# Kernel optimization log

Measured on AMD Instinct MI355X. Metric: run time of the kernel, lower is better.

Reference implementation:

```python
import jax, jax.numpy as jnp
import numpy as np

SENSOR_H, SENSOR_W = 256, 256
SPP = 16
BATCH, C, H_IMG, W_IMG = 4, 3, 1024, 1024


def setup_inputs() -> dict:
    key = jax.random.key(0)
    k1, k2 = jax.random.split(key)
    img = jax.random.uniform(k1, (BATCH, C, H_IMG, W_IMG), dtype=jnp.float32)
    jitter = jax.random.uniform(k2, (SPP, SENSOR_H, SENSOR_W, 2), dtype=jnp.float32)
    t = jnp.ones((1,), jnp.float32)
    return {"img": img, "t": t, "jitter": jitter}


def deform(pos, t):
    # Analytic per-axis foveation diffeomorphism [-1,1]^2 -> [-1,1]^2:
    #   f(u) = tanh(t*u)/tanh(t), f'(u) = t*(1 - tanh(t*u)^2)/tanh(t)
    # Jacobian is diagonal, so det = f'(x) * f'(y).
    tt = t[0]
    s = jnp.tanh(tt)
    th = jnp.tanh(tt * pos)
    warped = th / s                      # (..., 2)
    dd = tt * (1.0 - th * th) / s        # diagonal Jacobian entries (..., 2)
    det = dd[..., 0] * dd[..., 1]        # (...)
    return warped, det


def grid_sample_border(img, grid):
    # img: (b,c,H,W); grid: (spp,h,w,2) in [-1,1]
    # bilinear, padding_mode='border', align_corners=False (matches F.grid_sample)
    b, c, H, W = img.shape
    gx = (grid[..., 0] + 1.0) * (W / 2.0) - 0.5
    gy = (grid[..., 1] + 1.0) * (H / 2.0) - 0.5
    gx = jnp.clip(gx, 0.0, W - 1.0)
    gy = jnp.clip(gy, 0.0, H - 1.0)
    x0 = jnp.floor(gx)
    y0 = jnp.floor(gy)
    wx = (gx - x0)[None, None]           # (1,1,spp,h,w)
    wy = (gy - y0)[None, None]
    x0i = jnp.clip(x0.astype(jnp.int32), 0, W - 1)
    y0i = jnp.clip(y0.astype(jnp.int32), 0, H - 1)
    x1i = jnp.clip(x0i + 1, 0, W - 1)
    y1i = jnp.clip(y0i + 1, 0, H - 1)
    # fancy-index gather: result (b,c,spp,h,w); avoids tiling img over (b*spp)
    v00 = img[:, :, y0i, x0i]
    v01 = img[:, :, y0i, x1i]
    v10 = img[:, :, y1i, x0i]
    v11 = img[:, :, y1i, x1i]
    return (v00 * (1 - wx) * (1 - wy) + v01 * wx * (1 - wy)
            + v10 * (1 - wx) * wy + v11 * wx * wy)


def reference(img, t, jitter):
    step_x = 2.0 / SENSOR_W
    step_y = 2.0 / SENSOR_H
    px = jnp.arange(-1.0, 1.0, step_x, dtype=jnp.float32)
    py = jnp.arange(-1.0, 1.0, step_y, dtype=jnp.float32)
    gx, gy = jnp.meshgrid(px, py, indexing='xy')          # (h, w)
    pixel_pos = jnp.stack((gx, gy), axis=-1)[None]        # (1, h, w, 2)
    jit = jitter * jnp.array([step_x, step_y], jnp.float32)
    pos = pixel_pos + jit                                 # (spp, h, w, 2)
    warped, det = deform(pos, t)                          # (spp,h,w,2), (spp,h,w)
    samples = grid_sample_border(img, warped)             # (b, c, spp, h, w)
    weighted = jnp.mean(samples * det[None, None], axis=2)  # (b, c, h, w)
    area = jnp.mean(det, axis=0)[None, None]              # (1, 1, h, w)
    return weighted / area
```

## Files before the change

### kernel.cpp

```cpp
#include <hip/hip_runtime.h>
#include <hip/hip_fp16.h>

#define SPP   16
#define SH    256
#define SW    256
#define HI    1024
#define WI    1024
#define CH    3
#define BATCH 4

#define TS    4
#define MAXD  26
#define PLN   704
#define NITER 11
#define NTHR  128

#define AS1C(p) ((const __attribute__((address_space(1))) void*)(p))
#define AS3(p)  ((__attribute__((address_space(3))) void*)(p))

__device__ __forceinline__ float fast_tanh(float x) {
    const float e = __expf(2.0f * x);
    return (e - 1.0f) * __builtin_amdgcn_rcpf(e + 1.0f);
}

__global__ __launch_bounds__(NTHR, 6) void foveated_async4(
    const float* __restrict__ img,
    const float* __restrict__ t_ptr,
    const float* __restrict__ jitter,
    float* __restrict__ out)
{
    __shared__ float lds_f[2][CH][PLN];

    const int bid  = blockIdx.x;
    const int Lb   = (bid & 7) * 1024 + (bid >> 3);
    const int th   = threadIdx.x;
    const int w    = th >> 6;
    const int lane = th & 63;

    const int tile = Lb * 2 + w;
    const int b    = tile >> 12;
    const int rem  = tile & 4095;
    const int trow = rem >> 6;
    const int tcol = rem & 63;
    const int sx0  = tcol * TS;
    const int sy0  = trow * TS;

    const float step  = 2.0f / 256.0f;
    const float tt    = t_ptr[0];
    const float inv_s = __builtin_amdgcn_rcpf(fast_tanh(tt));

    auto gmap = [&](float p) {
        float g = (fast_tanh(tt * p) * inv_s + 1.0f) * 512.0f - 0.5f;
        return fminf(fmaxf(g, 0.0f), 1023.0f);
    };
    const float pxmin = -1.0f + sx0 * step, pxmax = pxmin + TS * step;
    const float pymin = -1.0f + sy0 * step, pymax = pymin + TS * step;
    const int x_lo = max((int)gmap(pxmin) - 1, 0);
    const int x_hi = min((int)gmap(pxmax) + 2, WI - 1);
    const int y_lo = max((int)gmap(pymin) - 1, 0);
    const int y_hi = min((int)gmap(pymax) + 2, HI - 1);
    const int ncols = x_hi - x_lo + 1;
    const int nrows = y_hi - y_lo + 1;
    const bool fits = (ncols > 0) && (nrows > 0) &&
                      (ncols <= MAXD) && (nrows <= MAXD);

    const size_t plane = (size_t)HI * WI;
    const float* __restrict__ p0 = img + (size_t)(b * CH) * plane;
    const float* __restrict__ p1 = p0 + plane;
    const float* __restrict__ p2 = p1 + plane;

    const int p  = lane >> 2;
    const int q  = lane & 3;
    const int sx = sx0 + (p & 3);
    const int sy = sy0 + (p >> 2);

    const float px = -1.0f + sx * step;
    const float py = -1.0f + sy * step;

    const float2* __restrict__ jit2 = (const float2*)jitter;
    const int jbase = (q * 4) * (SH * SW) + sy * SW + sx;
    const float2 jv0 = jit2[jbase];
    const float2 jv1 = jit2[jbase + 1 * (SH * SW)];
    const float2 jv2 = jit2[jbase + 2 * (SH * SW)];
    const float2 jv3 = jit2[jbase + 3 * (SH * SW)];

    float acc0 = 0.0f, acc1 = 0.0f, acc2 = 0.0f, dsum = 0.0f;

    float* __restrict__ P0 = &lds_f[w][0][0];
    float* __restrict__ P1 = &lds_f[w][1][0];
    float* __restrict__ P2 = &lds_f[w][2][0];

    auto sample_lds = [&](float jx, float jy) {
        const float posx = px + jx * step;
        const float posy = py + jy * step;

        const float thx = fast_tanh(tt * posx);
        const float thy = fast_tanh(tt * posy);
        const float ddx = tt * (1.0f - thx * thx) * inv_s;
        const float ddy = tt * (1.0f - thy * thy) * inv_s;
        const float det = ddx * ddy;

        float gx = (thx * inv_s + 1.0f) * 512.0f - 0.5f;
        float gy = (thy * inv_s + 1.0f) * 512.0f - 0.5f;
        gx = fminf(fmaxf(gx, 0.0f), (float)(WI - 1));
        gy = fminf(fmaxf(gy, 0.0f), (float)(HI - 1));

        const int xb = min((int)gx, WI - 2);
        const int yb = min((int)gy, HI - 2);
        const float fx = gx - (float)xb;
        const float fy = gy - (float)yb;

        const float w00 = (1.0f - fx) * (1.0f - fy) * det;
        const float w01 = fx * (1.0f - fy) * det;
        const float w10 = (1.0f - fx) * fy * det;
        const float w11 = fx * fy * det;
        dsum += det;

        const int lidx = (yb - y_lo) * ncols + (xb - x_lo);
        const int l01  = lidx + 1;
        const int l10  = lidx + ncols;
        const int l11  = l10 + 1;

        acc0 += w00 * P0[lidx] + w01 * P0[l01] + w10 * P0[l10] + w11 * P0[l11];
        acc1 += w00 * P1[lidx] + w01 * P1[l01] + w10 * P1[l10] + w11 * P1[l11];
        acc2 += w00 * P2[lidx] + w01 * P2[l01] + w10 * P2[l10] + w11 * P2[l11];
    };

    auto sample_glb = [&](float jx, float jy) {
        const float posx = px + jx * step;
        const float posy = py + jy * step;

        const float thx = fast_tanh(tt * posx);
        const float thy = fast_tanh(tt * posy);
        const float ddx = tt * (1.0f - thx * thx) * inv_s;
        const float ddy = tt * (1.0f - thy * thy) * inv_s;
        const float det = ddx * ddy;

        float gx = (thx * inv_s + 1.0f) * 512.0f - 0.5f;
        float gy = (thy * inv_s + 1.0f) * 512.0f - 0.5f;
        gx = fminf(fmaxf(gx, 0.0f), (float)(WI - 1));
        gy = fminf(fmaxf(gy, 0.0f), (float)(HI - 1));

        const int xb = min((int)gx, WI - 2);
        const int yb = min((int)gy, HI - 2);
        const float fx = gx - (float)xb;
        const float fy = gy - (float)yb;

        const float w00 = (1.0f - fx) * (1.0f - fy) * det;
        const float w01 = fx * (1.0f - fy) * det;
        const float w10 = (1.0f - fx) * fy * det;
        const float w11 = fx * fy * det;
        dsum += det;

        const int i0 = yb * WI + xb;
        const int i1 = i0 + WI;
        { const float a0 = p0[i0], a1 = p0[i0 + 1], c0 = p0[i1], c1 = p0[i1 + 1];
          acc0 += a0 * w00 + a1 * w01 + c0 * w10 + c1 * w11; }
        { const float a0 = p1[i0], a1 = p1[i0 + 1], c0 = p1[i1], c1 = p1[i1 + 1];
          acc1 += a0 * w00 + a1 * w01 + c0 * w10 + c1 * w11; }
        { const float a0 = p2[i0], a1 = p2[i0 + 1], c0 = p2[i1], c1 = p2[i1 + 1];
          acc2 += a0 * w00 + a1 * w01 + c0 * w10 + c1 * w11; }
    };

    if (fits) {
        const int npix  = nrows * ncols;
        const int niter = (npix + 63) >> 6;
        const unsigned mdiv = (1u << 22) / (unsigned)ncols + 1u;
        #pragma unroll
        for (int k = 0; k < NITER; ++k) {
            if (k < niter) {
                int i = k * 64 + lane;
                i = min(i, npix - 1);
                const int r = (int)(((unsigned)i * mdiv) >> 22);
                const int c = i - r * ncols;
                const int g = (y_lo + r) * WI + (x_lo + c);
                __builtin_amdgcn_global_load_lds(AS1C(p0 + g), AS3(P0 + k * 64), 4, 0, 0);
                __builtin_amdgcn_global_load_lds(AS1C(p1 + g), AS3(P1 + k * 64), 4, 0, 0);
                __builtin_amdgcn_global_load_lds(AS1C(p2 + g), AS3(P2 + k * 64), 4, 0, 0);
            }
        }
        asm volatile("s_waitcnt vmcnt(0)" ::: "memory");
        __builtin_amdgcn_sched_barrier(0);

        sample_lds(jv0.x, jv0.y);
        sample_lds(jv1.x, jv1.y);
        sample_lds(jv2.x, jv2.y);
        sample_lds(jv3.x, jv3.y);
    } else {
        sample_glb(jv0.x, jv0.y);
        sample_glb(jv1.x, jv1.y);
        sample_glb(jv2.x, jv2.y);
        sample_glb(jv3.x, jv3.y);
    }

    acc0 += __shfl_xor(acc0, 1);  acc0 += __shfl_xor(acc0, 2);
    acc1 += __shfl_xor(acc1, 1);  acc1 += __shfl_xor(acc1, 2);
    acc2 += __shfl_xor(acc2, 1);  acc2 += __shfl_xor(acc2, 2);
    dsum += __shfl_xor(dsum, 1);  dsum += __shfl_xor(dsum, 2);

    if (q == 0) {
        const float inv_d = 1.0f / dsum;
        const int pix = sy * SW + sx;
        const size_t ob = (size_t)b * CH * (SH * SW) + pix;
        out[ob]                 = acc0 * inv_d;
        out[ob + (SH * SW)]     = acc1 * inv_d;
        out[ob + 2 * (SH * SW)] = acc2 * inv_d;
    }
}

extern "C" void kernel_launch(void* const* d_in, const int* in_sizes, int n_in,
                              void* d_out, int out_size, void* d_ws, size_t ws_size,
                              hipStream_t stream) {
    const float* img    = (const float*)d_in[0];
    const float* t      = (const float*)d_in[1];
    const float* jitter = (const float*)d_in[2];
    float* out          = (float*)d_out;

    hipLaunchKernelGGL(foveated_async4, dim3(8192), dim3(NTHR), 0, stream,
                       img, t, jitter, out);
}
```

Baseline: 107.0 us.

## Use 8x8 sensor tiles per wave with one thread per pixel

Each block is now a single wave that covers an 8x8 sensor tile and computes all 16 samples per thread, where before each wave had a 4x4 tile with four lanes splitting the samples. Larger tiles make the staged LDS footprint smaller relative to the pixels covered, so fewer image texels are loaded twice across neighbouring tiles. The cross-lane shuffle reduction is gone. In exchange, the staging loop grows to 34 iterations, each thread holds more registers for the 16 jitter values, LDS use per block rises, and occupancy may drop.

New measurement: 103.5 us (median of 2 runs). -3.3%, faster.

```diff
diff --git a/kernel.cpp b/kernel.cpp
--- a/kernel.cpp
+++ b/kernel.cpp
@@ -9,11 +9,11 @@
 #define CH    3
 #define BATCH 4
 
-#define TS    4
-#define MAXD  26
-#define PLN   704
-#define NITER 11
-#define NTHR  128
+#define TS    8
+#define MAXD  46
+#define PLN   2176
+#define NITER 34
+#define NTHR  64
 
 #define AS1C(p) ((const __attribute__((address_space(1))) void*)(p))
 #define AS3(p)  ((__attribute__((address_space(3))) void*)(p))
@@ -23,27 +23,26 @@
     return (e - 1.0f) * __builtin_amdgcn_rcpf(e + 1.0f);
 }
 
-__global__ __launch_bounds__(NTHR, 6) void foveated_async4(
+__global__ __launch_bounds__(NTHR, 4) void foveated_wave8(
     const float* __restrict__ img,
     const float* __restrict__ t_ptr,
     const float* __restrict__ jitter,
     float* __restrict__ out)
 {
-    __shared__ float lds_f[2][CH][PLN];
+    __shared__ float lds_f[CH][PLN];
 
     const int bid  = blockIdx.x;
-    const int Lb   = (bid & 7) * 1024 + (bid >> 3);
-    const int th   = threadIdx.x;
-    const int w    = th >> 6;
-    const int lane = th & 63;
-
-    const int tile = Lb * 2 + w;
-    const int b    = tile >> 12;
-    const int rem  = tile & 4095;
-    const int trow = rem >> 6;
-    const int tcol = rem & 63;
+    const int L    = (bid & 7) * 512 + (bid >> 3);
+    const int b    = L >> 10;
+    const int rem  = L & 1023;
+    const int trow = rem >> 5;
+    const int tcol = rem & 31;
     const int sx0  = tcol * TS;
     const int sy0  = trow * TS;
+
+    const int lane = threadIdx.x;
+    const int sx   = sx0 + (lane & 7);
+    const int sy   = sy0 + (lane >> 3);
 
     const float step  = 2.0f / 256.0f;
     const float tt    = t_ptr[0];
@@ -69,26 +68,33 @@
     const float* __restrict__ p1 = p0 + plane;
     const float* __restrict__ p2 = p1 + plane;
 
-    const int p  = lane >> 2;
-    const int q  = lane & 3;
-    const int sx = sx0 + (p & 3);
-    const int sy = sy0 + (p >> 2);
-
     const float px = -1.0f + sx * step;
     const float py = -1.0f + sy * step;
 
     const float2* __restrict__ jit2 = (const float2*)jitter;
-    const int jbase = (q * 4) * (SH * SW) + sy * SW + sx;
-    const float2 jv0 = jit2[jbase];
-    const float2 jv1 = jit2[jbase + 1 * (SH * SW)];
-    const float2 jv2 = jit2[jbase + 2 * (SH * SW)];
-    const float2 jv3 = jit2[jbase + 3 * (SH * SW)];
+    const int jbase = sy * SW + sx;
+    const float2 jv0  = jit2[jbase +  0 * (SH * SW)];
+    const float2 jv1  = jit2[jbase +  1 * (SH * SW)];
+    const float2 jv2  = jit2[jbase +  2 * (SH * SW)];
+    const float2 jv3  = jit2[jbase +  3 * (SH * SW)];
+    const float2 jv4  = jit2[jbase +  4 * (SH * SW)];
+    const float2 jv5  = jit2[jbase +  5 * (SH * SW)];
+    const float2 jv6  = jit2[jbase +  6 * (SH * SW)];
+    const float2 jv7  = jit2[jbase +  7 * (SH * SW)];
+    const float2 jv8  = jit2[jbase +  8 * (SH * SW)];
+    const float2 jv9  = jit2[jbase +  9 * (SH * SW)];
+    const float2 jv10 = jit2[jbase + 10 * (SH * SW)];
+    const float2 jv11 = jit2[jbase + 11 * (SH * SW)];
+    const float2 jv12 = jit2[jbase + 12 * (SH * SW)];
+    const float2 jv13 = jit2[jbase + 13 * (SH * SW)];
+    const float2 jv14 = jit2[jbase + 14 * (SH * SW)];
+    const float2 jv15 = jit2[jbase + 15 * (SH * SW)];
 
     float acc0 = 0.0f, acc1 = 0.0f, acc2 = 0.0f, dsum = 0.0f;
 
-    float* __restrict__ P0 = &lds_f[w][0][0];
-    float* __restrict__ P1 = &lds_f[w][1][0];
-    float* __restrict__ P2 = &lds_f[w][2][0];
+    float* __restrict__ P0 = &lds_f[0][0];
+    float* __restrict__ P1 = &lds_f[1][0];
+    float* __restrict__ P2 = &lds_f[2][0];
 
     auto sample_lds = [&](float jx, float jy) {
         const float posx = px + jx * step;
@@ -117,13 +123,11 @@
         dsum += det;
 
         const int lidx = (yb - y_lo) * ncols + (xb - x_lo);
-        const int l01  = lidx + 1;
         const int l10  = lidx + ncols;
-        const int l11  = l10 + 1;
-
-        acc0 += w00 * P0[lidx] + w01 * P0[l01] + w10 * P0[l10] + w11 * P0[l11];
-        acc1 += w00 * P1[lidx] + w01 * P1[l01] + w10 * P1[l10] + w11 * P1[l11];
-        acc2 += w00 * P2[lidx] + w01 * P2[l01] + w10 * P2[l10] + w11 * P2[l11];
+
+        acc0 += w00 * P0[lidx] + w01 * P0[lidx + 1] + w10 * P0[l10] + w11 * P0[l10 + 1];
+        acc1 += w00 * P1[lidx] + w01 * P1[lidx + 1] + w10 * P1[l10] + w11 * P1[l10 + 1];
+        acc2 += w00 * P2[lidx] + w01 * P2[lidx + 1] + w10 * P2[l10] + w11 * P2[l10 + 1];
     };
 
     auto sample_glb = [&](float jx, float jy) {
@@ -182,30 +186,31 @@
         asm volatile("s_waitcnt vmcnt(0)" ::: "memory");
         __builtin_amdgcn_sched_barrier(0);
 
-        sample_lds(jv0.x, jv0.y);
-        sample_lds(jv1.x, jv1.y);
-        sample_lds(jv2.x, jv2.y);
-        sample_lds(jv3.x, jv3.y);
+        sample_lds(jv0.x,  jv0.y);   sample_lds(jv1.x,  jv1.y);
+        sample_lds(jv2.x,  jv2.y);   sample_lds(jv3.x,  jv3.y);
+        sample_lds(jv4.x,  jv4.y);   sample_lds(jv5.x,  jv5.y);
+        sample_lds(jv6.x,  jv6.y);   sample_lds(jv7.x,  jv7.y);
+        sample_lds(jv8.x,  jv8.y);   sample_lds(jv9.x,  jv9.y);
+        sample_lds(jv10.x, jv10.y);  sample_lds(jv11.x, jv11.y);
+        sample_lds(jv12.x, jv12.y);  sample_lds(jv13.x, jv13.y);
+        sample_lds(jv14.x, jv14.y);  sample_lds(jv15.x, jv15.y);
     } else {
-        sample_glb(jv0.x, jv0.y);
-        sample_glb(jv1.x, jv1.y);
-        sample_glb(jv2.x, jv2.y);
-        sample_glb(jv3.x, jv3.y);
+        sample_glb(jv0.x,  jv0.y);   sample_glb(jv1.x,  jv1.y);
+        sample_glb(jv2.x,  jv2.y);   sample_glb(jv3.x,  jv3.y);
+        sample_glb(jv4.x,  jv4.y);   sample_glb(jv5.x,  jv5.y);
+        sample_glb(jv6.x,  jv6.y);   sample_glb(jv7.x,  jv7.y);
+        sample_glb(jv8.x,  jv8.y);   sample_glb(jv9.x,  jv9.y);
+        sample_glb(jv10.x, jv10.y);  sample_glb(jv11.x, jv11.y);
+        sample_glb(jv12.x, jv12.y);  sample_glb(jv13.x, jv13.y);
+        sample_glb(jv14.x, jv14.y);  sample_glb(jv15.x, jv15.y);
     }
 
-    acc0 += __shfl_xor(acc0, 1);  acc0 += __shfl_xor(acc0, 2);
-    acc1 += __shfl_xor(acc1, 1);  acc1 += __shfl_xor(acc1, 2);
-    acc2 += __shfl_xor(acc2, 1);  acc2 += __shfl_xor(acc2, 2);
-    dsum += __shfl_xor(dsum, 1);  dsum += __shfl_xor(dsum, 2);
-
-    if (q == 0) {
-        const float inv_d = 1.0f / dsum;
-        const int pix = sy * SW + sx;
-        const size_t ob = (size_t)b * CH * (SH * SW) + pix;
-        out[ob]                 = acc0 * inv_d;
-        out[ob + (SH * SW)]     = acc1 * inv_d;
-        out[ob + 2 * (SH * SW)] = acc2 * inv_d;
-    }
+    const float inv_d = 1.0f / dsum;
+    const int pix = sy * SW + sx;
+    const size_t ob = (size_t)b * CH * (SH * SW) + pix;
+    out[ob]                 = acc0 * inv_d;
+    out[ob + (SH * SW)]     = acc1 * inv_d;
+    out[ob + 2 * (SH * SW)] = acc2 * inv_d;
 }
 
 extern "C" void kernel_launch(void* const* d_in, const int* in_sizes, int n_in,
@@ -216,6 +221,6 @@
     const float* jitter = (const float*)d_in[2];
     float* out          = (float*)d_out;
 
-    hipLaunchKernelGGL(foveated_async4, dim3(8192), dim3(NTHR), 0, stream,
+    hipLaunchKernelGGL(foveated_wave8, dim3(4096), dim3(NTHR), 0, stream,
                        img, t, jitter, out);
 }
```
